# Optimization experiments

Hardware: AMD Instinct MI355X
Metric: run time of the kernel (lower is better)

The kernel has to match this reference:

```python
import jax, jax.numpy as jnp
import numpy as np

NG = 64            # init arg ng
OMEGA_V = 1.0      # self.Omega (undefined in source; treated as constant)
TILDE_OMEGA_V = 2.0  # self.tilde_Omega
RTOL, ATOL = 1e-5, 1e-8  # torch.allclose defaults


def setup_inputs() -> dict:
    key = jax.random.key(0)
    k = jax.random.split(key, 6)
    nq = nm = 128
    nkappa, d, ng = 16, 48, NG
    q = jax.random.normal(k[0], (nq, 3), jnp.float32)
    omega = jax.random.uniform(k[1], (nm,), jnp.float32)
    e_tilde = jax.random.normal(k[2], (3, nkappa, nm, nq, d), jnp.float32)
    e = jax.random.normal(k[3], (3, nkappa, d, ng, nq), jnp.float32)
    g_vecs = jax.random.normal(k[4], (ng, 3), jnp.float32)
    G_vec = jax.random.normal(k[5], (3,), jnp.float32)
    # Q chosen so each q-point matches the unfolding condition for g index 0
    Q = q + g_vecs[0] - G_vec
    return {"q": q, "omega": omega, "e_tilde": e_tilde, "e": e,
            "g_vecs": g_vecs, "G_vec": G_vec, "Q": Q}


def reference(q, omega, e_tilde, e, g_vecs, G_vec, Q):
    nq = q.shape[0]
    nm = omega.shape[0]
    # allclose(Q[i], q[i] + g[j] - G) -> boolean mask [nq, ng]
    unfolded = q[:, None, :] + g_vecs[None, :, :] - G_vec  # [nq, ng, 3]
    mask = jnp.all(jnp.abs(Q[:, None, :] - unfolded) <= ATOL + RTOL * jnp.abs(unfolded), axis=-1)
    # dot over eigenvector dim d for every (alpha, kappa, mode, q-point, g)
    dots = jnp.einsum('akmid,akdgi->akmig', e_tilde, e)  # [3, nkappa, nm, nq, ng]
    w = jnp.sum(jnp.abs(dots) ** 2, axis=(0, 1))          # [nm, nq, ng]
    # accumulate only where the unfolding condition holds, then normalize
    P = jnp.einsum('mig,ig->im', w, mask.astype(w.dtype)) * (OMEGA_V / TILDE_OMEGA_V / NG)  # [nq, nm]
    # A[i, mu] = sum_k P[k, mu] * eq(omega[k], omega[mu])  (independent of i)
    E = (omega[:, None] == omega[None, :]).astype(P.dtype)  # [nm, nm]
    A_mu = jnp.einsum('mk,km->m', E, P)
    return jnp.broadcast_to(A_mu, (nq, nm))
```

## Files before the change

### kernel.cpp

```cpp
#include <hip/hip_runtime.h>

#define NQ   128
#define NM   128
#define ND   48
#define NGV  64
#define NAK  48
#define RTOL_C 1e-5f
#define ATOL_C 1e-8f
#define SCALE_C (1.0f / 128.0f)

typedef float f32x4 __attribute__((ext_vector_type(4)));

__global__ __launch_bounds__(256) void k_prep(
    const float* __restrict__ q, const float* __restrict__ gv,
    const float* __restrict__ G, const float* __restrict__ Q,
    unsigned long long* __restrict__ mbits, float* __restrict__ P)
{
    int gid = blockIdx.x * 256 + threadIdx.x;
    if (gid < NQ * NM) P[gid] = 0.0f;
    if (gid < NQ) {
        int i = gid;
        float qx = q[i*3+0], qy = q[i*3+1], qz = q[i*3+2];
        float Qx = Q[i*3+0], Qy = Q[i*3+1], Qz = Q[i*3+2];
        float Gx = G[0], Gy = G[1], Gz = G[2];
        unsigned long long bits = 0ull;
        for (int g = 0; g < NGV; ++g) {
            float ux = qx + gv[g*3+0] - Gx;
            float uy = qy + gv[g*3+1] - Gy;
            float uz = qz + gv[g*3+2] - Gz;
            bool ok = (fabsf(Qx - ux) <= ATOL_C + RTOL_C * fabsf(ux)) &&
                      (fabsf(Qy - uy) <= ATOL_C + RTOL_C * fabsf(uy)) &&
                      (fabsf(Qz - uz) <= ATOL_C + RTOL_C * fabsf(uz));
            if (ok) bits |= (1ull << g);
        }
        mbits[i] = bits;
    }
}

__global__ __launch_bounds__(256) void k_main(
    const float* __restrict__ et,
    const float* __restrict__ e,
    const unsigned long long* __restrict__ mbits,
    float* __restrict__ P)
{
    int bid   = blockIdx.x;
    int m     = bid >> 3;
    int itile = (bid >> 2) & 1;
    int chunk = bid & 3;

    int tid = threadIdx.x;
    int grp = tid >> 2;
    int sub = tid & 3;
    int i   = itile * 64 + grp;
    int d0  = sub * 12;

    unsigned long long mb = mbits[i];
    float acc = 0.0f;

#pragma unroll 2
    for (int akx = 0; akx < 12; ++akx) {
        int ak = chunk * 12 + akx;
        const float* rowt = et + ((((size_t)ak * NM + m) * NQ + i) * ND + d0);
        f32x4 t0 = __builtin_nontemporal_load(reinterpret_cast<const f32x4*>(rowt + 0));
        f32x4 t1 = __builtin_nontemporal_load(reinterpret_cast<const f32x4*>(rowt + 4));
        f32x4 t2 = __builtin_nontemporal_load(reinterpret_cast<const f32x4*>(rowt + 8));

        const float* ep = e + (((size_t)ak * ND + d0) * NGV * NQ + i);

        unsigned long long mm = mb;
        while (mm) {
            int g = __ffsll(mm) - 1;
            mm &= (mm - 1);
            const float* eg = ep + (size_t)g * NQ;
            float dot;
            dot  = t0.x * eg[0*8192] + t0.y * eg[1*8192];
            dot += t0.z * eg[2*8192] + t0.w * eg[3*8192];
            dot += t1.x * eg[4*8192] + t1.y * eg[5*8192];
            dot += t1.z * eg[6*8192] + t1.w * eg[7*8192];
            dot += t2.x * eg[8*8192] + t2.y * eg[9*8192];
            dot += t2.z * eg[10*8192] + t2.w * eg[11*8192];
            dot += __shfl_xor(dot, 1, 4);
            dot += __shfl_xor(dot, 2, 4);
            acc += dot * dot;
        }
    }

    if (sub == 0) {
        atomicAdd(&P[(size_t)i * NM + m], acc * SCALE_C);
    }
}

__global__ __launch_bounds__(256) void k_final(
    const float* __restrict__ omega, const float* __restrict__ P,
    float* __restrict__ out)
{
    __shared__ float A[NM];
    int tid = threadIdx.x;
    if (tid < NM) {
        float om  = omega[tid];
        float acc = 0.0f;
        for (int k = 0; k < NM; ++k) {
            if (omega[k] == om) acc += P[(size_t)k * NM + tid];
        }
        A[tid] = acc;
    }
    __syncthreads();
    int base = blockIdx.x * 512;
    for (int idx = tid; idx < 512; idx += 256) {
        int o = base + idx;
        out[o] = A[o & (NM - 1)];
    }
}

extern "C" void kernel_launch(void* const* d_in, const int* in_sizes, int n_in,
                              void* d_out, int out_size, void* d_ws, size_t ws_size,
                              hipStream_t stream)
{
    const float* q     = (const float*)d_in[0];
    const float* omega = (const float*)d_in[1];
    const float* et    = (const float*)d_in[2];
    const float* e     = (const float*)d_in[3];
    const float* gv    = (const float*)d_in[4];
    const float* G     = (const float*)d_in[5];
    const float* Q     = (const float*)d_in[6];
    float* out = (float*)d_out;

    unsigned long long* mbits = (unsigned long long*)d_ws;
    float* P = (float*)((char*)d_ws + 4096);

    k_prep<<<64, 256, 0, stream>>>(q, gv, G, Q, mbits, P);
    k_main<<<1024, 256, 0, stream>>>(et, e, mbits, P);
    k_final<<<32, 256, 0, stream>>>(omega, P, out);
}
```

Measured before the change: 296.9 us.

## Gather masked e columns into contiguous d-major buffer before main dot kernel

Result: faster. 286.2 us (-3.6%).

```diff
diff --git a/kernel.cpp b/kernel.cpp
--- a/kernel.cpp
+++ b/kernel.cpp
@@ -11,10 +11,16 @@
 
 typedef float f32x4 __attribute__((ext_vector_type(4)));
 
+#define WS_GLIST   0
+#define WS_GCOUNT  8192
+#define WS_P       16384
+#define WS_EC      (1u << 20)
+
 __global__ __launch_bounds__(256) void k_prep(
     const float* __restrict__ q, const float* __restrict__ gv,
     const float* __restrict__ G, const float* __restrict__ Q,
-    unsigned long long* __restrict__ mbits, float* __restrict__ P)
+    unsigned char* __restrict__ glist, int* __restrict__ gcount,
+    float* __restrict__ P)
 {
     int gid = blockIdx.x * 256 + threadIdx.x;
     if (gid < NQ * NM) P[gid] = 0.0f;
@@ -23,7 +29,7 @@
         float qx = q[i*3+0], qy = q[i*3+1], qz = q[i*3+2];
         float Qx = Q[i*3+0], Qy = Q[i*3+1], Qz = Q[i*3+2];
         float Gx = G[0], Gy = G[1], Gz = G[2];
-        unsigned long long bits = 0ull;
+        int cnt = 0;
         for (int g = 0; g < NGV; ++g) {
             float ux = qx + gv[g*3+0] - Gx;
             float uy = qy + gv[g*3+1] - Gy;
@@ -31,16 +37,34 @@
             bool ok = (fabsf(Qx - ux) <= ATOL_C + RTOL_C * fabsf(ux)) &&
                       (fabsf(Qy - uy) <= ATOL_C + RTOL_C * fabsf(uy)) &&
                       (fabsf(Qz - uz) <= ATOL_C + RTOL_C * fabsf(uz));
-            if (ok) bits |= (1ull << g);
+            if (ok) { glist[i*NGV + cnt] = (unsigned char)g; ++cnt; }
         }
-        mbits[i] = bits;
+        gcount[i] = cnt;
+    }
+}
+
+__global__ __launch_bounds__(256) void k_gather(
+    const float* __restrict__ e,
+    const unsigned char* __restrict__ glist,
+    const int* __restrict__ gcount,
+    float* __restrict__ ec)
+{
+    int t = blockIdx.x * 256 + threadIdx.x;
+    int i  = t & (NQ - 1);
+    int d  = (t >> 7) % ND;
+    int ak = t / (NQ * ND);
+    int gc = gcount[i];
+    for (int s = 0; s < gc; ++s) {
+        int g = glist[i*NGV + s];
+        float v = e[(((size_t)ak * ND + d) * NGV + g) * NQ + i];
+        ec[(((size_t)s * NAK + ak) * NQ + i) * ND + d] = v;
     }
 }
 
 __global__ __launch_bounds__(256) void k_main(
     const float* __restrict__ et,
-    const float* __restrict__ e,
-    const unsigned long long* __restrict__ mbits,
+    const float* __restrict__ ec,
+    const int* __restrict__ gcount,
     float* __restrict__ P)
 {
     int bid   = blockIdx.x;
@@ -49,36 +73,29 @@
     int chunk = bid & 3;
 
     int tid = threadIdx.x;
-    int grp = tid >> 2;
+    int i   = itile * 64 + (tid >> 2);
     int sub = tid & 3;
-    int i   = itile * 64 + grp;
     int d0  = sub * 12;
 
-    unsigned long long mb = mbits[i];
+    int gc = gcount[i];
     float acc = 0.0f;
 
-#pragma unroll 2
     for (int akx = 0; akx < 12; ++akx) {
         int ak = chunk * 12 + akx;
         const float* rowt = et + ((((size_t)ak * NM + m) * NQ + i) * ND + d0);
-        f32x4 t0 = __builtin_nontemporal_load(reinterpret_cast<const f32x4*>(rowt + 0));
-        f32x4 t1 = __builtin_nontemporal_load(reinterpret_cast<const f32x4*>(rowt + 4));
-        f32x4 t2 = __builtin_nontemporal_load(reinterpret_cast<const f32x4*>(rowt + 8));
+        f32x4 t0 = *reinterpret_cast<const f32x4*>(rowt + 0);
+        f32x4 t1 = *reinterpret_cast<const f32x4*>(rowt + 4);
+        f32x4 t2 = *reinterpret_cast<const f32x4*>(rowt + 8);
 
-        const float* ep = e + (((size_t)ak * ND + d0) * NGV * NQ + i);
-
-        unsigned long long mm = mb;
-        while (mm) {
-            int g = __ffsll(mm) - 1;
-            mm &= (mm - 1);
-            const float* eg = ep + (size_t)g * NQ;
+        for (int s = 0; s < gc; ++s) {
+            const float* rowc = ec + ((((size_t)s * NAK + ak) * NQ + i) * ND + d0);
+            f32x4 c0 = *reinterpret_cast<const f32x4*>(rowc + 0);
+            f32x4 c1 = *reinterpret_cast<const f32x4*>(rowc + 4);
+            f32x4 c2 = *reinterpret_cast<const f32x4*>(rowc + 8);
             float dot;
-            dot  = t0.x * eg[0*8192] + t0.y * eg[1*8192];
-            dot += t0.z * eg[2*8192] + t0.w * eg[3*8192];
-            dot += t1.x * eg[4*8192] + t1.y * eg[5*8192];
-            dot += t1.z * eg[6*8192] + t1.w * eg[7*8192];
-            dot += t2.x * eg[8*8192] + t2.y * eg[9*8192];
-            dot += t2.z * eg[10*8192] + t2.w * eg[11*8192];
+            dot  = t0.x*c0.x + t0.y*c0.y + t0.z*c0.z + t0.w*c0.w;
+            dot += t1.x*c1.x + t1.y*c1.y + t1.z*c1.z + t1.w*c1.w;
+            dot += t2.x*c2.x + t2.y*c2.y + t2.z*c2.z + t2.w*c2.w;
             dot += __shfl_xor(dot, 1, 4);
             dot += __shfl_xor(dot, 2, 4);
             acc += dot * dot;
@@ -125,10 +142,13 @@
     const float* Q     = (const float*)d_in[6];
     float* out = (float*)d_out;
 
-    unsigned long long* mbits = (unsigned long long*)d_ws;
-    float* P = (float*)((char*)d_ws + 4096);
+    unsigned char* glist  = (unsigned char*)d_ws + WS_GLIST;
+    int*           gcount = (int*)((char*)d_ws + WS_GCOUNT);
+    float*         P      = (float*)((char*)d_ws + WS_P);
+    float*         ec     = (float*)((char*)d_ws + WS_EC);
 
-    k_prep<<<64, 256, 0, stream>>>(q, gv, G, Q, mbits, P);
-    k_main<<<1024, 256, 0, stream>>>(et, e, mbits, P);
-    k_final<<<32, 256, 0, stream>>>(omega, P, out);
+    k_prep  <<<64,   256, 0, stream>>>(q, gv, G, Q, glist, gcount, P);
+    k_gather<<<1152, 256, 0, stream>>>(e, glist, gcount, ec);
+    k_main  <<<1024, 256, 0, stream>>>(et, ec, gcount, P);
+    k_final <<<32,   256, 0, stream>>>(omega, P, out);
 }
```
